# Optimization experiments

Measured on AMD Instinct MI355X. Metric: run time of the kernel, lower is better.

The kernel has to match this reference:

```python
import jax, jax.numpy as jnp
import numpy as np

N_SRC = 100000
N_DST = 50000
N_EDGES = 600000
D = 128


def setup_inputs() -> dict:
    key = jax.random.key(0)
    k1, k2, k3, k4, k5 = jax.random.split(key, 5)
    src_rep = jax.random.normal(k1, (N_SRC, D), dtype=jnp.float32)
    dst_rep = jax.random.normal(k2, (N_DST, D), dtype=jnp.float32)
    edge_src = jax.random.randint(k3, (N_EDGES,), 0, N_SRC, dtype=jnp.int64)
    edge_dst = jax.random.randint(k4, (N_EDGES,), 0, N_DST, dtype=jnp.int64)
    W = jax.random.normal(k5, (2 * D, D), dtype=jnp.float32) * (1.0 / np.sqrt(2 * D))
    b = jnp.zeros((D,), dtype=jnp.float32)
    return {"src_rep": src_rep, "dst_rep": dst_rep, "edge_src": edge_src,
            "edge_dst": edge_dst, "W": W, "b": b}


def reference(src_rep, dst_rep, edge_src, edge_dst, W, b):
    # copy_src: gather source reps along edges  [E, D]
    msgs = src_rep[edge_src]
    # sum reduce: scatter-add messages to destination nodes  [N_dst, D]
    agg = jax.ops.segment_sum(msgs, edge_dst, num_segments=dst_rep.shape[0])
    # NodeUpdater: concat(dst rep, summed messages) -> Linear -> activation
    # (Dropout is identity in eval mode.)
    concat = jnp.concatenate([dst_rep, agg], axis=1)  # [N_dst, 2D]
    new_rep = jax.nn.relu(concat @ W + b)  # [N_dst, D]
    return new_rep
```

## Files before the change

kernel.cpp:

```cpp
#include <hip/hip_runtime.h>

#define N_SRC   100000
#define N_DST   50000
#define N_EDGES 600000
#define D       128
#define RPB     16
#define PAD     48

#define CONV_THREADS ((N_SRC * D) / 8)
#define CONV_BLOCKS  (CONV_THREADS / 256)
#define FILL_BLOCKS  ((N_EDGES + 255) / 256)

typedef short bf16x8 __attribute__((ext_vector_type(8)));
typedef float f32x4  __attribute__((ext_vector_type(4)));

static __device__ __forceinline__ unsigned short f2bf(float f) {
    unsigned u = __float_as_uint(f);
    u += 0x7FFF + ((u >> 16) & 1);
    return (unsigned short)(u >> 16);
}
static __device__ __forceinline__ unsigned pk(float a, float b) {
    return (unsigned)f2bf(a) | ((unsigned)f2bf(b) << 16);
}
static __device__ __forceinline__ void addpk(float* a, uint4 u) {
    a[0] += __uint_as_float(u.x << 16);
    a[1] += __uint_as_float(u.x & 0xFFFF0000u);
    a[2] += __uint_as_float(u.y << 16);
    a[3] += __uint_as_float(u.y & 0xFFFF0000u);
    a[4] += __uint_as_float(u.z << 16);
    a[5] += __uint_as_float(u.z & 0xFFFF0000u);
    a[6] += __uint_as_float(u.w << 16);
    a[7] += __uint_as_float(u.w & 0xFFFF0000u);
}

__global__ __launch_bounds__(256) void prep_kernel(
    const float* __restrict__ W, unsigned short* __restrict__ Wt,
    int* __restrict__ cnt) {
    int t = blockIdx.x * 256 + threadIdx.x;
    if (t < 2 * D * D) {
        int n = t >> 8, k = t & 255;
        Wt[n * 256 + k] = f2bf(W[(size_t)k * D + n]);
    }
    int c = t - 2 * D * D;
    if (c >= 0 && c < N_DST) cnt[c] = 0;
}

__global__ __launch_bounds__(256) void convfill_kernel(
    const float* __restrict__ src_rep, unsigned short* __restrict__ srcb,
    const int* __restrict__ edge_src, const int* __restrict__ edge_dst,
    int* __restrict__ cnt, int* __restrict__ perm) {
    if (blockIdx.x < CONV_BLOCKS) {
        int t = blockIdx.x * 256 + threadIdx.x;
        const float4* p = reinterpret_cast<const float4*>(src_rep) + (size_t)t * 2;
        float4 v0 = p[0], v1 = p[1];
        uint4 w;
        w.x = pk(v0.x, v0.y); w.y = pk(v0.z, v0.w);
        w.z = pk(v1.x, v1.y); w.w = pk(v1.z, v1.w);
        reinterpret_cast<uint4*>(srcb)[t] = w;
    } else {
        int e = (blockIdx.x - CONV_BLOCKS) * 256 + threadIdx.x;
        if (e < N_EDGES) {
            int d = edge_dst[e];
            int pos = atomicAdd(&cnt[d], 1);
            if (pos < PAD) perm[d * PAD + pos] = edge_src[e];
        }
    }
}

__global__ __launch_bounds__(256) void fill_kernel(
    const int* __restrict__ edge_src, const int* __restrict__ edge_dst,
    int* __restrict__ cnt, int* __restrict__ perm) {
    int e = blockIdx.x * 256 + threadIdx.x;
    if (e < N_EDGES) {
        int d = edge_dst[e];
        int pos = atomicAdd(&cnt[d], 1);
        if (pos < PAD) perm[d * PAD + pos] = edge_src[e];
    }
}

__global__ __launch_bounds__(256) void gather_bf16_kernel(
    const unsigned short* __restrict__ srcb,
    const int* __restrict__ cnt,
    const int* __restrict__ perm,
    unsigned short* __restrict__ agg) {
    const int tid = threadIdx.x, lane = tid & 63, wave = tid >> 6;
    const int q = lane >> 4, cl = lane & 15;
    const int dn = blockIdx.x * 4 + wave;
    const int deg = min(cnt[dn], PAD);
    const int pi = perm[(size_t)dn * PAD + min(lane, PAD - 1)];
    const int dm1 = deg - 1;

    float a0[8] = {0,0,0,0,0,0,0,0}, a1[8] = {0,0,0,0,0,0,0,0};
    for (int base = 0; base < deg; base += 16) {
        int e0 = base + q, e1 = base + 4 + q, e2 = base + 8 + q, e3 = base + 12 + q;
        int s0 = __shfl(pi, min(e0, dm1));
        int s1 = __shfl(pi, min(e1, dm1));
        int s2 = __shfl(pi, min(e2, dm1));
        int s3 = __shfl(pi, min(e3, dm1));
        uint4 u0 = {0,0,0,0}, u1 = {0,0,0,0}, u2 = {0,0,0,0}, u3 = {0,0,0,0};
        if (e0 <= dm1) u0 = *reinterpret_cast<const uint4*>(srcb + (size_t)s0 * D + cl * 8);
        if (e1 <= dm1) u1 = *reinterpret_cast<const uint4*>(srcb + (size_t)s1 * D + cl * 8);
        if (e2 <= dm1) u2 = *reinterpret_cast<const uint4*>(srcb + (size_t)s2 * D + cl * 8);
        if (e3 <= dm1) u3 = *reinterpret_cast<const uint4*>(srcb + (size_t)s3 * D + cl * 8);
        addpk(a0, u0); addpk(a1, u1); addpk(a0, u2); addpk(a1, u3);
    }
#pragma unroll
    for (int i = 0; i < 8; ++i) {
        a0[i] += a1[i];
        a0[i] += __shfl_xor(a0[i], 16);
        a0[i] += __shfl_xor(a0[i], 32);
    }
    if (lane < 16) {
        uint4 w;
        w.x = pk(a0[0], a0[1]); w.y = pk(a0[2], a0[3]);
        w.z = pk(a0[4], a0[5]); w.w = pk(a0[6], a0[7]);
        *reinterpret_cast<uint4*>(agg + (size_t)dn * D + cl * 8) = w;
    }
}

__global__ __launch_bounds__(256) void gather_f32_kernel(
    const float* __restrict__ src_rep,
    const int*   __restrict__ cnt,
    const int*   __restrict__ perm,
    unsigned short* __restrict__ agg) {
    const int tid = threadIdx.x, lane = tid & 63, wave = tid >> 6;
    const int h = lane >> 5, c = lane & 31;
    const int dn = blockIdx.x * 4 + wave;
    const int deg = min(cnt[dn], PAD);
    const int pi = perm[(size_t)dn * PAD + min(lane, PAD - 1)];

    f32x4 a0 = {0.f, 0.f, 0.f, 0.f}, a1 = a0, a2 = a0, a3 = a0;
    const int dm1 = deg - 1;
    for (int base = 0; base < deg; base += 8) {
        int e0 = base + h, e1 = base + 2 + h, e2 = base + 4 + h, e3 = base + 6 + h;
        int s0 = __shfl(pi, min(e0, dm1));
        int s1 = __shfl(pi, min(e1, dm1));
        int s2 = __shfl(pi, min(e2, dm1));
        int s3 = __shfl(pi, min(e3, dm1));
        if (e0 <= dm1) a0 += *reinterpret_cast<const f32x4*>(src_rep + (size_t)s0 * D + c * 4);
        if (e1 <= dm1) a1 += *reinterpret_cast<const f32x4*>(src_rep + (size_t)s1 * D + c * 4);
        if (e2 <= dm1) a2 += *reinterpret_cast<const f32x4*>(src_rep + (size_t)s2 * D + c * 4);
        if (e3 <= dm1) a3 += *reinterpret_cast<const f32x4*>(src_rep + (size_t)s3 * D + c * 4);
    }
    a0 += a1; a2 += a3; a0 += a2;
#pragma unroll
    for (int qq = 0; qq < 4; ++qq) a0[qq] += __shfl_xor(a0[qq], 32);
    if (h == 0) {
        uint2 w;
        w.x = pk(a0[0], a0[1]); w.y = pk(a0[2], a0[3]);
        *reinterpret_cast<uint2*>(agg + (size_t)dn * D + c * 4) = w;
    }
}

__global__ __launch_bounds__(256) void gemm_kernel(
    const float* __restrict__ dst_rep,
    const unsigned short* __restrict__ agg,
    const unsigned short* __restrict__ Wt,
    const float* __restrict__ bias,
    float*       __restrict__ out) {
    __shared__ unsigned short Abf[RPB * 2 * D];
    const int row0 = blockIdx.x * RPB;
    const int tid = threadIdx.x, lane = tid & 63, wave = tid >> 6;

    {
        int r = tid >> 4, b = tid & 15;
        const float4* p = reinterpret_cast<const float4*>(
            dst_rep + (size_t)(row0 + r) * D + b * 8);
        float4 v0 = p[0], v1 = p[1];
        uint4 w;
        w.x = pk(v0.x, v0.y); w.y = pk(v0.z, v0.w);
        w.z = pk(v1.x, v1.y); w.w = pk(v1.z, v1.w);
        *reinterpret_cast<uint4*>(&Abf[r * 256 + (b ^ (r & 7)) * 8]) = w;
        uint4 g = *reinterpret_cast<const uint4*>(agg + (size_t)(row0 + r) * D + b * 8);
        *reinterpret_cast<uint4*>(&Abf[r * 256 + ((16 + b) ^ (r & 7)) * 8]) = g;
    }
    __syncthreads();

    f32x4 c0 = {0.f, 0.f, 0.f, 0.f}, c1 = {0.f, 0.f, 0.f, 0.f};
    const int ar = lane & 15;
    const int kb = lane >> 4;
    const int n0 = wave * 32 + (lane & 15);
#pragma unroll
    for (int s = 0; s < 8; ++s) {
        int b = s * 4 + kb;
        bf16x8 af = *reinterpret_cast<const bf16x8*>(&Abf[ar * 256 + (b ^ (ar & 7)) * 8]);
        int kbase = s * 32 + kb * 8;
        bf16x8 b0 = *reinterpret_cast<const bf16x8*>(&Wt[(size_t)n0 * 256 + kbase]);
        bf16x8 b1 = *reinterpret_cast<const bf16x8*>(&Wt[(size_t)(n0 + 16) * 256 + kbase]);
        c0 = __builtin_amdgcn_mfma_f32_16x16x32_bf16(af, b0, c0, 0, 0, 0);
        c1 = __builtin_amdgcn_mfma_f32_16x16x32_bf16(af, b1, c1, 0, 0, 0);
    }

    const float bv0 = bias[wave * 32 + (lane & 15)];
    const float bv1 = bias[wave * 32 + 16 + (lane & 15)];
#pragma unroll
    for (int g = 0; g < 4; ++g) {
        size_t orow = row0 + (lane >> 4) * 4 + g;
        out[orow * D + wave * 32 + (lane & 15)]      = fmaxf(c0[g] + bv0, 0.f);
        out[orow * D + wave * 32 + 16 + (lane & 15)] = fmaxf(c1[g] + bv1, 0.f);
    }
}

extern "C" void kernel_launch(void* const* d_in, const int* in_sizes, int n_in,
                              void* d_out, int out_size, void* d_ws, size_t ws_size,
                              hipStream_t stream) {
    const float* src_rep  = (const float*)d_in[0];
    const float* dst_rep  = (const float*)d_in[1];
    const int*   edge_src = (const int*)d_in[2];
    const int*   edge_dst = (const int*)d_in[3];
    const float* W        = (const float*)d_in[4];
    const float* bias     = (const float*)d_in[5];
    float*       out      = (float*)d_out;

    int* cnt  = (int*)d_ws;
    int* perm = cnt + N_DST;
    size_t wt_off = (((size_t)N_DST * (1 + PAD) * 4 + 255) / 256) * 256;
    unsigned short* Wt   = (unsigned short*)((char*)d_ws + wt_off);
    unsigned short* agg  = Wt + (size_t)2 * D * D;
    unsigned short* srcb = agg + (size_t)N_DST * D;
    const size_t need_full = wt_off + ((size_t)2 * D * D + (size_t)N_DST * D
                             + (size_t)N_SRC * D) * sizeof(unsigned short);

    prep_kernel<<<(2 * D * D + N_DST + 255) / 256, 256, 0, stream>>>(W, Wt, cnt);
    if (ws_size >= need_full) {
        convfill_kernel<<<CONV_BLOCKS + FILL_BLOCKS, 256, 0, stream>>>(
            src_rep, srcb, edge_src, edge_dst, cnt, perm);
        gather_bf16_kernel<<<N_DST / 4, 256, 0, stream>>>(srcb, cnt, perm, agg);
    } else {
        fill_kernel<<<FILL_BLOCKS, 256, 0, stream>>>(edge_src, edge_dst, cnt, perm);
        gather_f32_kernel<<<N_DST / 4, 256, 0, stream>>>(src_rep, cnt, perm, agg);
    }
    gemm_kernel<<<N_DST / RPB, 256, 0, stream>>>(dst_rep, agg, Wt, bias, out);
}
```

Baseline: 118.6 us.

## Fuse gather-sum into GEMM kernel and merge bf16 conversion with prep

The neighbor gather-sum and the linear+ReLU GEMM now run in one 512-thread kernel. Eight waves aggregate two destination rows each directly into shared memory, so the bf16 agg buffer is never written to or read back from global memory. The src_rep bf16 conversion now sits in the same launch as the W transpose and count zeroing, and the edge fill gets its own launch. This trades one kernel boundary and an agg round trip for a serialized gather-then-MFMA phase inside each block, with one MFMA column tile per wave.

Measured after the change: 98.20 us. -17.2%, faster.

```diff
diff --git a/kernel.cpp b/kernel.cpp
--- a/kernel.cpp
+++ b/kernel.cpp
@@ -7,8 +7,9 @@
 #define RPB     16
 #define PAD     48
 
-#define CONV_THREADS ((N_SRC * D) / 8)
-#define CONV_BLOCKS  (CONV_THREADS / 256)
+#define CONV_BLOCKS  ((N_SRC * D / 4) / 256)
+#define MISC_ELEMS   (2 * D * D + N_DST)
+#define MISC_BLOCKS  ((MISC_ELEMS + 255) / 256)
 #define FILL_BLOCKS  ((N_EDGES + 255) / 256)
 
 typedef short bf16x8 __attribute__((ext_vector_type(8)));
@@ -34,36 +35,23 @@
 }
 
 __global__ __launch_bounds__(256) void prep_kernel(
+    const float* __restrict__ src_rep, unsigned short* __restrict__ srcb,
     const float* __restrict__ W, unsigned short* __restrict__ Wt,
     int* __restrict__ cnt) {
-    int t = blockIdx.x * 256 + threadIdx.x;
-    if (t < 2 * D * D) {
-        int n = t >> 8, k = t & 255;
-        Wt[n * 256 + k] = f2bf(W[(size_t)k * D + n]);
-    }
-    int c = t - 2 * D * D;
-    if (c >= 0 && c < N_DST) cnt[c] = 0;
-}
-
-__global__ __launch_bounds__(256) void convfill_kernel(
-    const float* __restrict__ src_rep, unsigned short* __restrict__ srcb,
-    const int* __restrict__ edge_src, const int* __restrict__ edge_dst,
-    int* __restrict__ cnt, int* __restrict__ perm) {
     if (blockIdx.x < CONV_BLOCKS) {
-        int t = blockIdx.x * 256 + threadIdx.x;
-        const float4* p = reinterpret_cast<const float4*>(src_rep) + (size_t)t * 2;
-        float4 v0 = p[0], v1 = p[1];
-        uint4 w;
-        w.x = pk(v0.x, v0.y); w.y = pk(v0.z, v0.w);
-        w.z = pk(v1.x, v1.y); w.w = pk(v1.z, v1.w);
-        reinterpret_cast<uint4*>(srcb)[t] = w;
+        size_t t = (size_t)blockIdx.x * 256 + threadIdx.x;
+        float4 v = reinterpret_cast<const float4*>(src_rep)[t];
+        uint2 w;
+        w.x = pk(v.x, v.y); w.y = pk(v.z, v.w);
+        reinterpret_cast<uint2*>(srcb)[t] = w;
     } else {
-        int e = (blockIdx.x - CONV_BLOCKS) * 256 + threadIdx.x;
-        if (e < N_EDGES) {
-            int d = edge_dst[e];
-            int pos = atomicAdd(&cnt[d], 1);
-            if (pos < PAD) perm[d * PAD + pos] = edge_src[e];
-        }
+        int t = (blockIdx.x - CONV_BLOCKS) * 256 + threadIdx.x;
+        if (t < 2 * D * D) {
+            int n = t >> 8, k = t & 255;
+            Wt[n * 256 + k] = f2bf(W[(size_t)k * D + n]);
+        }
+        int c = t - 2 * D * D;
+        if (c >= 0 && c < N_DST) cnt[c] = 0;
     }
 }
 
@@ -78,44 +66,96 @@
     }
 }
 
-__global__ __launch_bounds__(256) void gather_bf16_kernel(
+__global__ __launch_bounds__(512) void fused_kernel(
     const unsigned short* __restrict__ srcb,
-    const int* __restrict__ cnt,
-    const int* __restrict__ perm,
-    unsigned short* __restrict__ agg) {
+    const float* __restrict__ dst_rep,
+    const int*   __restrict__ cnt,
+    const int*   __restrict__ perm,
+    const unsigned short* __restrict__ Wt,
+    const float* __restrict__ bias,
+    float*       __restrict__ out) {
+    __shared__ unsigned short Abf[16 * 2 * D];
+    const int row0 = blockIdx.x * 16;
     const int tid = threadIdx.x, lane = tid & 63, wave = tid >> 6;
     const int q = lane >> 4, cl = lane & 15;
-    const int dn = blockIdx.x * 4 + wave;
-    const int deg = min(cnt[dn], PAD);
-    const int pi = perm[(size_t)dn * PAD + min(lane, PAD - 1)];
-    const int dm1 = deg - 1;
-
-    float a0[8] = {0,0,0,0,0,0,0,0}, a1[8] = {0,0,0,0,0,0,0,0};
-    for (int base = 0; base < deg; base += 16) {
-        int e0 = base + q, e1 = base + 4 + q, e2 = base + 8 + q, e3 = base + 12 + q;
-        int s0 = __shfl(pi, min(e0, dm1));
-        int s1 = __shfl(pi, min(e1, dm1));
-        int s2 = __shfl(pi, min(e2, dm1));
-        int s3 = __shfl(pi, min(e3, dm1));
-        uint4 u0 = {0,0,0,0}, u1 = {0,0,0,0}, u2 = {0,0,0,0}, u3 = {0,0,0,0};
-        if (e0 <= dm1) u0 = *reinterpret_cast<const uint4*>(srcb + (size_t)s0 * D + cl * 8);
-        if (e1 <= dm1) u1 = *reinterpret_cast<const uint4*>(srcb + (size_t)s1 * D + cl * 8);
-        if (e2 <= dm1) u2 = *reinterpret_cast<const uint4*>(srcb + (size_t)s2 * D + cl * 8);
-        if (e3 <= dm1) u3 = *reinterpret_cast<const uint4*>(srcb + (size_t)s3 * D + cl * 8);
-        addpk(a0, u0); addpk(a1, u1); addpk(a0, u2); addpk(a1, u3);
-    }
-#pragma unroll
-    for (int i = 0; i < 8; ++i) {
-        a0[i] += a1[i];
-        a0[i] += __shfl_xor(a0[i], 16);
-        a0[i] += __shfl_xor(a0[i], 32);
-    }
-    if (lane < 16) {
+
+    if (tid < 256) {
+        int r = tid >> 4, b = tid & 15;
+        const float4* p = reinterpret_cast<const float4*>(
+            dst_rep + (size_t)(row0 + r) * D + b * 8);
+        float4 v0 = p[0], v1 = p[1];
         uint4 w;
-        w.x = pk(a0[0], a0[1]); w.y = pk(a0[2], a0[3]);
-        w.z = pk(a0[4], a0[5]); w.w = pk(a0[6], a0[7]);
-        *reinterpret_cast<uint4*>(agg + (size_t)dn * D + cl * 8) = w;
-    }
+        w.x = pk(v0.x, v0.y); w.y = pk(v0.z, v0.w);
+        w.z = pk(v1.x, v1.y); w.w = pk(v1.z, v1.w);
+        *reinterpret_cast<uint4*>(&Abf[r * 256 + (b ^ (r & 7)) * 8]) = w;
+    }
+
+#pragma unroll
+    for (int rr = 0; rr < 2; ++rr) {
+        const int r  = wave * 2 + rr;
+        const int dn = row0 + r;
+        const int deg = min(cnt[dn], PAD);
+        const int pi = perm[(size_t)dn * PAD + min(lane, PAD - 1)];
+        const int dm1 = deg - 1;
+        float a0[8] = {0,0,0,0,0,0,0,0}, a1[8] = {0,0,0,0,0,0,0,0};
+        for (int base = 0; base < deg; base += 16) {
+            int e0 = base + q, e1 = base + 4 + q, e2 = base + 8 + q, e3 = base + 12 + q;
+            int s0 = __shfl(pi, min(e0, dm1));
+            int s1 = __shfl(pi, min(e1, dm1));
+            int s2 = __shfl(pi, min(e2, dm1));
+            int s3 = __shfl(pi, min(e3, dm1));
+            uint4 u0 = {0,0,0,0}, u1 = {0,0,0,0}, u2 = {0,0,0,0}, u3 = {0,0,0,0};
+            if (e0 <= dm1) u0 = *reinterpret_cast<const uint4*>(srcb + (size_t)s0 * D + cl * 8);
+            if (e1 <= dm1) u1 = *reinterpret_cast<const uint4*>(srcb + (size_t)s1 * D + cl * 8);
+            if (e2 <= dm1) u2 = *reinterpret_cast<const uint4*>(srcb + (size_t)s2 * D + cl * 8);
+            if (e3 <= dm1) u3 = *reinterpret_cast<const uint4*>(srcb + (size_t)s3 * D + cl * 8);
+            addpk(a0, u0); addpk(a1, u1); addpk(a0, u2); addpk(a1, u3);
+        }
+#pragma unroll
+        for (int i = 0; i < 8; ++i) {
+            a0[i] += a1[i];
+            a0[i] += __shfl_xor(a0[i], 16);
+            a0[i] += __shfl_xor(a0[i], 32);
+        }
+        if (lane < 16) {
+            uint4 w;
+            w.x = pk(a0[0], a0[1]); w.y = pk(a0[2], a0[3]);
+            w.z = pk(a0[4], a0[5]); w.w = pk(a0[6], a0[7]);
+            *reinterpret_cast<uint4*>(&Abf[r * 256 + ((16 + cl) ^ (r & 7)) * 8]) = w;
+        }
+    }
+    __syncthreads();
+
+    f32x4 c0 = {0.f, 0.f, 0.f, 0.f};
+    const int ar = lane & 15;
+    const int kb = lane >> 4;
+    const int n0 = wave * 16 + (lane & 15);
+#pragma unroll
+    for (int s = 0; s < 8; ++s) {
+        int b = s * 4 + kb;
+        bf16x8 af = *reinterpret_cast<const bf16x8*>(&Abf[ar * 256 + (b ^ (ar & 7)) * 8]);
+        bf16x8 b0 = *reinterpret_cast<const bf16x8*>(&Wt[(size_t)n0 * 256 + s * 32 + kb * 8]);
+        c0 = __builtin_amdgcn_mfma_f32_16x16x32_bf16(af, b0, c0, 0, 0, 0);
+    }
+
+    const float bv = bias[n0];
+#pragma unroll
+    for (int g = 0; g < 4; ++g) {
+        size_t orow = row0 + (lane >> 4) * 4 + g;
+        out[orow * D + n0] = fmaxf(c0[g] + bv, 0.f);
+    }
+}
+
+__global__ __launch_bounds__(256) void prep_small_kernel(
+    const float* __restrict__ W, unsigned short* __restrict__ Wt,
+    int* __restrict__ cnt) {
+    int t = blockIdx.x * 256 + threadIdx.x;
+    if (t < 2 * D * D) {
+        int n = t >> 8, k = t & 255;
+        Wt[n * 256 + k] = f2bf(W[(size_t)k * D + n]);
+    }
+    int c = t - 2 * D * D;
+    if (c >= 0 && c < N_DST) cnt[c] = 0;
 }
 
 __global__ __launch_bounds__(256) void gather_f32_kernel(
@@ -161,7 +201,6 @@
     __shared__ unsigned short Abf[RPB * 2 * D];
     const int row0 = blockIdx.x * RPB;
     const int tid = threadIdx.x, lane = tid & 63, wave = tid >> 6;
-
     {
         int r = tid >> 4, b = tid & 15;
         const float4* p = reinterpret_cast<const float4*>(
@@ -190,7 +229,6 @@
         c0 = __builtin_amdgcn_mfma_f32_16x16x32_bf16(af, b0, c0, 0, 0, 0);
         c1 = __builtin_amdgcn_mfma_f32_16x16x32_bf16(af, b1, c1, 0, 0, 0);
     }
-
     const float bv0 = bias[wave * 32 + (lane & 15)];
     const float bv1 = bias[wave * 32 + 16 + (lane & 15)];
 #pragma unroll
@@ -216,19 +254,22 @@
     int* perm = cnt + N_DST;
     size_t wt_off = (((size_t)N_DST * (1 + PAD) * 4 + 255) / 256) * 256;
     unsigned short* Wt   = (unsigned short*)((char*)d_ws + wt_off);
-    unsigned short* agg  = Wt + (size_t)2 * D * D;
-    unsigned short* srcb = agg + (size_t)N_DST * D;
-    const size_t need_full = wt_off + ((size_t)2 * D * D + (size_t)N_DST * D
-                             + (size_t)N_SRC * D) * sizeof(unsigned short);
-
-    prep_kernel<<<(2 * D * D + N_DST + 255) / 256, 256, 0, stream>>>(W, Wt, cnt);
+    unsigned short* big  = Wt + (size_t)2 * D * D;
+    const size_t need_full = wt_off + ((size_t)2 * D * D + (size_t)N_SRC * D)
+                             * sizeof(unsigned short);
+
     if (ws_size >= need_full) {
-        convfill_kernel<<<CONV_BLOCKS + FILL_BLOCKS, 256, 0, stream>>>(
-            src_rep, srcb, edge_src, edge_dst, cnt, perm);
-        gather_bf16_kernel<<<N_DST / 4, 256, 0, stream>>>(srcb, cnt, perm, agg);
+        unsigned short* srcb = big;
+        prep_kernel<<<CONV_BLOCKS + MISC_BLOCKS, 256, 0, stream>>>(
+            src_rep, srcb, W, Wt, cnt);
+        fill_kernel<<<FILL_BLOCKS, 256, 0, stream>>>(edge_src, edge_dst, cnt, perm);
+        fused_kernel<<<N_DST / 16, 512, 0, stream>>>(
+            srcb, dst_rep, cnt, perm, Wt, bias, out);
     } else {
+        unsigned short* agg = big;
+        prep_small_kernel<<<MISC_BLOCKS, 256, 0, stream>>>(W, Wt, cnt);
         fill_kernel<<<FILL_BLOCKS, 256, 0, stream>>>(edge_src, edge_dst, cnt, perm);
         gather_f32_kernel<<<N_DST / 4, 256, 0, stream>>>(src_rep, cnt, perm, agg);
-    }
-    gemm_kernel<<<N_DST / RPB, 256, 0, stream>>>(dst_rep, agg, Wt, bias, out);
-}
+        gemm_kernel<<<N_DST / RPB, 256, 0, stream>>>(dst_rep, agg, Wt, bias, out);
+    }
+}
```

## Gather neighbor rows via direct global-to-LDS loads and regroup prep kernels

Applied to the files above, without the earlier changes.

The bf16 gather kernel now issues global_load_lds transfers into a per-wave LDS staging buffer, with out-of-range edges pointed at a zero row appended to srcb. The partial sums are then read back from LDS and accumulated. The src conversion moves into the prep kernel together with the W transpose and count reset, using a float4-per-thread conversion, and fill becomes a separate launch. The aim is to issue gather loads with fewer VGPRs and without branches, in exchange for a full vmcnt wait every iteration and an extra kernel launch.

Result: faster. 106.7 us (-10.0%).

```diff
diff --git a/kernel.cpp b/kernel.cpp
--- a/kernel.cpp
+++ b/kernel.cpp
@@ -7,8 +7,9 @@
 #define RPB     16
 #define PAD     48
 
-#define CONV_THREADS ((N_SRC * D) / 8)
-#define CONV_BLOCKS  (CONV_THREADS / 256)
+#define CONV_BLOCKS  ((N_SRC * D / 4) / 256)
+#define MISC_ELEMS   (2 * D * D + N_DST + D)
+#define MISC_BLOCKS  ((MISC_ELEMS + 255) / 256)
 #define FILL_BLOCKS  ((N_EDGES + 255) / 256)
 
 typedef short bf16x8 __attribute__((ext_vector_type(8)));
@@ -34,36 +35,25 @@
 }
 
 __global__ __launch_bounds__(256) void prep_kernel(
+    const float* __restrict__ src_rep, unsigned short* __restrict__ srcb,
     const float* __restrict__ W, unsigned short* __restrict__ Wt,
     int* __restrict__ cnt) {
-    int t = blockIdx.x * 256 + threadIdx.x;
-    if (t < 2 * D * D) {
-        int n = t >> 8, k = t & 255;
-        Wt[n * 256 + k] = f2bf(W[(size_t)k * D + n]);
-    }
-    int c = t - 2 * D * D;
-    if (c >= 0 && c < N_DST) cnt[c] = 0;
-}
-
-__global__ __launch_bounds__(256) void convfill_kernel(
-    const float* __restrict__ src_rep, unsigned short* __restrict__ srcb,
-    const int* __restrict__ edge_src, const int* __restrict__ edge_dst,
-    int* __restrict__ cnt, int* __restrict__ perm) {
     if (blockIdx.x < CONV_BLOCKS) {
-        int t = blockIdx.x * 256 + threadIdx.x;
-        const float4* p = reinterpret_cast<const float4*>(src_rep) + (size_t)t * 2;
-        float4 v0 = p[0], v1 = p[1];
-        uint4 w;
-        w.x = pk(v0.x, v0.y); w.y = pk(v0.z, v0.w);
-        w.z = pk(v1.x, v1.y); w.w = pk(v1.z, v1.w);
-        reinterpret_cast<uint4*>(srcb)[t] = w;
+        size_t t = (size_t)blockIdx.x * 256 + threadIdx.x;
+        float4 v = reinterpret_cast<const float4*>(src_rep)[t];
+        uint2 w;
+        w.x = pk(v.x, v.y); w.y = pk(v.z, v.w);
+        reinterpret_cast<uint2*>(srcb)[t] = w;
     } else {
-        int e = (blockIdx.x - CONV_BLOCKS) * 256 + threadIdx.x;
-        if (e < N_EDGES) {
-            int d = edge_dst[e];
-            int pos = atomicAdd(&cnt[d], 1);
-            if (pos < PAD) perm[d * PAD + pos] = edge_src[e];
+        int t = (blockIdx.x - CONV_BLOCKS) * 256 + threadIdx.x;
+        if (t < 2 * D * D) {
+            int n = t >> 8, k = t & 255;
+            Wt[n * 256 + k] = f2bf(W[(size_t)k * D + n]);
         }
+        int c = t - 2 * D * D;
+        if (c >= 0 && c < N_DST) cnt[c] = 0;
+        int z = c - N_DST;
+        if (z >= 0 && z < D) srcb[(size_t)N_SRC * D + z] = 0;
     }
 }
 
@@ -78,77 +68,54 @@
     }
 }
 
-__global__ __launch_bounds__(256) void gather_bf16_kernel(
+__global__ __launch_bounds__(256) void gather_lds_kernel(
     const unsigned short* __restrict__ srcb,
     const int* __restrict__ cnt,
     const int* __restrict__ perm,
     unsigned short* __restrict__ agg) {
+    __shared__ __align__(16) unsigned short stage[4][2048];
     const int tid = threadIdx.x, lane = tid & 63, wave = tid >> 6;
     const int q = lane >> 4, cl = lane & 15;
     const int dn = blockIdx.x * 4 + wave;
     const int deg = min(cnt[dn], PAD);
     const int pi = perm[(size_t)dn * PAD + min(lane, PAD - 1)];
-    const int dm1 = deg - 1;
-
-    float a0[8] = {0,0,0,0,0,0,0,0}, a1[8] = {0,0,0,0,0,0,0,0};
+    const int dm = deg - 1, dc = max(dm, 0);
+    unsigned short* st = stage[wave];
+
+    float acc0[8] = {}, acc1[8] = {};
     for (int base = 0; base < deg; base += 16) {
-        int e0 = base + q, e1 = base + 4 + q, e2 = base + 8 + q, e3 = base + 12 + q;
-        int s0 = __shfl(pi, min(e0, dm1));
-        int s1 = __shfl(pi, min(e1, dm1));
-        int s2 = __shfl(pi, min(e2, dm1));
-        int s3 = __shfl(pi, min(e3, dm1));
-        uint4 u0 = {0,0,0,0}, u1 = {0,0,0,0}, u2 = {0,0,0,0}, u3 = {0,0,0,0};
-        if (e0 <= dm1) u0 = *reinterpret_cast<const uint4*>(srcb + (size_t)s0 * D + cl * 8);
-        if (e1 <= dm1) u1 = *reinterpret_cast<const uint4*>(srcb + (size_t)s1 * D + cl * 8);
-        if (e2 <= dm1) u2 = *reinterpret_cast<const uint4*>(srcb + (size_t)s2 * D + cl * 8);
-        if (e3 <= dm1) u3 = *reinterpret_cast<const uint4*>(srcb + (size_t)s3 * D + cl * 8);
-        addpk(a0, u0); addpk(a1, u1); addpk(a0, u2); addpk(a1, u3);
-    }
+#pragma unroll
+        for (int k = 0; k < 4; ++k) {
+            int e = base + 4 * k + q;
+            int row = __shfl(pi, min(e, dc));
+            row = (e <= dm) ? row : N_SRC;
+            __builtin_amdgcn_global_load_lds(
+                (const unsigned int*)(srcb + (size_t)row * D + cl * 8),
+                (unsigned int*)(st + k * 512), 16, 0, 0);
+        }
+        asm volatile("s_waitcnt vmcnt(0)" ::: "memory");
+        __builtin_amdgcn_sched_barrier(0);
+#pragma unroll
+        for (int k = 0; k < 4; ++k) {
+            uint4 u = *reinterpret_cast<const uint4*>(st + k * 512 + q * 128 + cl * 8);
+            addpk((k & 1) ? acc1 : acc0, u);
+        }
+        asm volatile("s_waitcnt lgkmcnt(0)" ::: "memory");
+        __builtin_amdgcn_sched_barrier(0);
+    }
+
 #pragma unroll
     for (int i = 0; i < 8; ++i) {
-        a0[i] += a1[i];
-        a0[i] += __shfl_xor(a0[i], 16);
-        a0[i] += __shfl_xor(a0[i], 32);
+        float s = acc0[i] + acc1[i];
+        s += __shfl_xor(s, 16);
+        s += __shfl_xor(s, 32);
+        acc0[i] = s;
     }
     if (lane < 16) {
         uint4 w;
-        w.x = pk(a0[0], a0[1]); w.y = pk(a0[2], a0[3]);
-        w.z = pk(a0[4], a0[5]); w.w = pk(a0[6], a0[7]);
+        w.x = pk(acc0[0], acc0[1]); w.y = pk(acc0[2], acc0[3]);
+        w.z = pk(acc0[4], acc0[5]); w.w = pk(acc0[6], acc0[7]);
         *reinterpret_cast<uint4*>(agg + (size_t)dn * D + cl * 8) = w;
-    }
-}
-
-__global__ __launch_bounds__(256) void gather_f32_kernel(
-    const float* __restrict__ src_rep,
-    const int*   __restrict__ cnt,
-    const int*   __restrict__ perm,
-    unsigned short* __restrict__ agg) {
-    const int tid = threadIdx.x, lane = tid & 63, wave = tid >> 6;
-    const int h = lane >> 5, c = lane & 31;
-    const int dn = blockIdx.x * 4 + wave;
-    const int deg = min(cnt[dn], PAD);
-    const int pi = perm[(size_t)dn * PAD + min(lane, PAD - 1)];
-
-    f32x4 a0 = {0.f, 0.f, 0.f, 0.f}, a1 = a0, a2 = a0, a3 = a0;
-    const int dm1 = deg - 1;
-    for (int base = 0; base < deg; base += 8) {
-        int e0 = base + h, e1 = base + 2 + h, e2 = base + 4 + h, e3 = base + 6 + h;
-        int s0 = __shfl(pi, min(e0, dm1));
-        int s1 = __shfl(pi, min(e1, dm1));
-        int s2 = __shfl(pi, min(e2, dm1));
-        int s3 = __shfl(pi, min(e3, dm1));
-        if (e0 <= dm1) a0 += *reinterpret_cast<const f32x4*>(src_rep + (size_t)s0 * D + c * 4);
-        if (e1 <= dm1) a1 += *reinterpret_cast<const f32x4*>(src_rep + (size_t)s1 * D + c * 4);
-        if (e2 <= dm1) a2 += *reinterpret_cast<const f32x4*>(src_rep + (size_t)s2 * D + c * 4);
-        if (e3 <= dm1) a3 += *reinterpret_cast<const f32x4*>(src_rep + (size_t)s3 * D + c * 4);
-    }
-    a0 += a1; a2 += a3; a0 += a2;
-#pragma unroll
-    for (int qq = 0; qq < 4; ++qq) a0[qq] += __shfl_xor(a0[qq], 32);
-    if (h == 0) {
-        uint2 w;
-        w.x = pk(a0[0], a0[1]); w.y = pk(a0[2], a0[3]);
-        *reinterpret_cast<uint2*>(agg + (size_t)dn * D + c * 4) = w;
     }
 }
 
@@ -161,7 +128,6 @@
     __shared__ unsigned short Abf[RPB * 2 * D];
     const int row0 = blockIdx.x * RPB;
     const int tid = threadIdx.x, lane = tid & 63, wave = tid >> 6;
-
     {
         int r = tid >> 4, b = tid & 15;
         const float4* p = reinterpret_cast<const float4*>(
@@ -190,7 +156,6 @@
         c0 = __builtin_amdgcn_mfma_f32_16x16x32_bf16(af, b0, c0, 0, 0, 0);
         c1 = __builtin_amdgcn_mfma_f32_16x16x32_bf16(af, b1, c1, 0, 0, 0);
     }
-
     const float bv0 = bias[wave * 32 + (lane & 15)];
     const float bv1 = bias[wave * 32 + 16 + (lane & 15)];
 #pragma unroll
@@ -198,6 +163,52 @@
         size_t orow = row0 + (lane >> 4) * 4 + g;
         out[orow * D + wave * 32 + (lane & 15)]      = fmaxf(c0[g] + bv0, 0.f);
         out[orow * D + wave * 32 + 16 + (lane & 15)] = fmaxf(c1[g] + bv1, 0.f);
+    }
+}
+
+__global__ __launch_bounds__(256) void prep_small_kernel(
+    const float* __restrict__ W, unsigned short* __restrict__ Wt,
+    int* __restrict__ cnt) {
+    int t = blockIdx.x * 256 + threadIdx.x;
+    if (t < 2 * D * D) {
+        int n = t >> 8, k = t & 255;
+        Wt[n * 256 + k] = f2bf(W[(size_t)k * D + n]);
+    }
+    int c = t - 2 * D * D;
+    if (c >= 0 && c < N_DST) cnt[c] = 0;
+}
+
+__global__ __launch_bounds__(256) void gather_f32_kernel(
+    const float* __restrict__ src_rep,
+    const int*   __restrict__ cnt,
+    const int*   __restrict__ perm,
+    unsigned short* __restrict__ agg) {
+    const int tid = threadIdx.x, lane = tid & 63, wave = tid >> 6;
+    const int h = lane >> 5, c = lane & 31;
+    const int dn = blockIdx.x * 4 + wave;
+    const int deg = min(cnt[dn], PAD);
+    const int pi = perm[(size_t)dn * PAD + min(lane, PAD - 1)];
+
+    f32x4 a0 = {0.f, 0.f, 0.f, 0.f}, a1 = a0, a2 = a0, a3 = a0;
+    const int dm1 = deg - 1;
+    for (int base = 0; base < deg; base += 8) {
+        int e0 = base + h, e1 = base + 2 + h, e2 = base + 4 + h, e3 = base + 6 + h;
+        int s0 = __shfl(pi, min(e0, max(dm1, 0)));
+        int s1 = __shfl(pi, min(e1, max(dm1, 0)));
+        int s2 = __shfl(pi, min(e2, max(dm1, 0)));
+        int s3 = __shfl(pi, min(e3, max(dm1, 0)));
+        if (e0 <= dm1) a0 += *reinterpret_cast<const f32x4*>(src_rep + (size_t)s0 * D + c * 4);
+        if (e1 <= dm1) a1 += *reinterpret_cast<const f32x4*>(src_rep + (size_t)s1 * D + c * 4);
+        if (e2 <= dm1) a2 += *reinterpret_cast<const f32x4*>(src_rep + (size_t)s2 * D + c * 4);
+        if (e3 <= dm1) a3 += *reinterpret_cast<const f32x4*>(src_rep + (size_t)s3 * D + c * 4);
+    }
+    a0 += a1; a2 += a3; a0 += a2;
+#pragma unroll
+    for (int qq = 0; qq < 4; ++qq) a0[qq] += __shfl_xor(a0[qq], 32);
+    if (h == 0) {
+        uint2 w;
+        w.x = pk(a0[0], a0[1]); w.y = pk(a0[2], a0[3]);
+        *reinterpret_cast<uint2*>(agg + (size_t)dn * D + c * 4) = w;
     }
 }
 
@@ -219,16 +230,18 @@
     unsigned short* agg  = Wt + (size_t)2 * D * D;
     unsigned short* srcb = agg + (size_t)N_DST * D;
     const size_t need_full = wt_off + ((size_t)2 * D * D + (size_t)N_DST * D
-                             + (size_t)N_SRC * D) * sizeof(unsigned short);
-
-    prep_kernel<<<(2 * D * D + N_DST + 255) / 256, 256, 0, stream>>>(W, Wt, cnt);
+                             + (size_t)(N_SRC + 1) * D) * sizeof(unsigned short);
+
     if (ws_size >= need_full) {
-        convfill_kernel<<<CONV_BLOCKS + FILL_BLOCKS, 256, 0, stream>>>(
-            src_rep, srcb, edge_src, edge_dst, cnt, perm);
-        gather_bf16_kernel<<<N_DST / 4, 256, 0, stream>>>(srcb, cnt, perm, agg);
+        prep_kernel<<<CONV_BLOCKS + MISC_BLOCKS, 256, 0, stream>>>(
+            src_rep, srcb, W, Wt, cnt);
+        fill_kernel<<<FILL_BLOCKS, 256, 0, stream>>>(edge_src, edge_dst, cnt, perm);
+        gather_lds_kernel<<<N_DST / 4, 256, 0, stream>>>(srcb, cnt, perm, agg);
+        gemm_kernel<<<N_DST / RPB, 256, 0, stream>>>(dst_rep, agg, Wt, bias, out);
     } else {
+        prep_small_kernel<<<MISC_BLOCKS, 256, 0, stream>>>(W, Wt, cnt);
         fill_kernel<<<FILL_BLOCKS, 256, 0, stream>>>(edge_src, edge_dst, cnt, perm);
         gather_f32_kernel<<<N_DST / 4, 256, 0, stream>>>(src_rep, cnt, perm, agg);
-    }
-    gemm_kernel<<<N_DST / RPB, 256, 0, stream>>>(dst_rep, agg, Wt, bias, out);
-}
+        gemm_kernel<<<N_DST / RPB, 256, 0, stream>>>(dst_rep, agg, Wt, bias, out);
+    }
+}
```
